# Performance work log

Measured on AMD Instinct MI355X. Metric: run time of the kernel, lower is better.

## Reference

```python
import jax, jax.numpy as jnp
import numpy as np

NUM_GRAPHS = 2048
NODES_PER_GRAPH = 16
EDGES_PER_GRAPH = 128
HEADS = 2
IN_CH = 256
HID_CH = 256
OUT_CH = 256
NEG_SLOPE = 0.2


def setup_inputs() -> dict:
    key = jax.random.key(0)
    ks = jax.random.split(key, 16)
    N = NUM_GRAPHS * NODES_PER_GRAPH
    E = NUM_GRAPHS * EDGES_PER_GRAPH
    x = jax.random.normal(ks[0], (N, IN_CH), dtype=jnp.float32)
    # intra-graph random edges: local indices + per-graph offsets
    offs = jnp.repeat(jnp.arange(NUM_GRAPHS, dtype=jnp.int64) * NODES_PER_GRAPH, EDGES_PER_GRAPH)
    src = jax.random.randint(ks[1], (E,), 0, NODES_PER_GRAPH, dtype=jnp.int64) + offs
    dst = jax.random.randint(ks[2], (E,), 0, NODES_PER_GRAPH, dtype=jnp.int64) + offs
    edge_index = jnp.stack([src, dst], axis=0)
    batch = jnp.repeat(jnp.arange(NUM_GRAPHS, dtype=jnp.int64), NODES_PER_GRAPH)
    s = 0.05
    return {
        'x': x,
        'edge_index': edge_index,
        'batch': batch,
        'W1': jax.random.normal(ks[3], (HEADS * HID_CH, IN_CH), dtype=jnp.float32) * s,
        'att_src1': jax.random.normal(ks[4], (HEADS, HID_CH), dtype=jnp.float32) * s,
        'att_dst1': jax.random.normal(ks[5], (HEADS, HID_CH), dtype=jnp.float32) * s,
        'b1': jax.random.normal(ks[6], (HID_CH,), dtype=jnp.float32) * s,
        'W2': jax.random.normal(ks[7], (HEADS * OUT_CH, HID_CH), dtype=jnp.float32) * s,
        'att_src2': jax.random.normal(ks[8], (HEADS, OUT_CH), dtype=jnp.float32) * s,
        'att_dst2': jax.random.normal(ks[9], (HEADS, OUT_CH), dtype=jnp.float32) * s,
        'b2': jax.random.normal(ks[10], (OUT_CH,), dtype=jnp.float32) * s,
        'w_att': jax.random.normal(ks[11], (OUT_CH, 1), dtype=jnp.float32) * s,
        'b_att': jax.random.normal(ks[12], (1,), dtype=jnp.float32) * s,
        'Wc': jax.random.normal(ks[13], (2, OUT_CH), dtype=jnp.float32) * s,
        'bc': jax.random.normal(ks[14], (2,), dtype=jnp.float32) * s,
    }


def _segment_softmax(logits, seg, num_seg):
    m = jax.ops.segment_max(logits, seg, num_segments=num_seg)
    e = jnp.exp(logits - m[seg])
    s = jax.ops.segment_sum(e, seg, num_segments=num_seg)
    return e / (s[seg] + 1e-16)


def _gat_conv(x, edge_index, W, a_src, a_dst, bias, out_ch):
    # PyG GATConv, heads=HEADS, concat=False, add_self_loops=True
    N = x.shape[0]
    h = (x @ W.T).reshape(N, HEADS, out_ch)              # [N,H,C]
    loop = jnp.arange(N, dtype=edge_index.dtype)
    src = jnp.concatenate([edge_index[0], loop])
    dst = jnp.concatenate([edge_index[1], loop])
    a_s = jnp.einsum('nhc,hc->nh', h, a_src)             # [N,H]
    a_d = jnp.einsum('nhc,hc->nh', h, a_dst)
    alpha = jax.nn.leaky_relu(a_s[src] + a_d[dst], NEG_SLOPE)  # [Etot,H]
    alpha = _segment_softmax(alpha, dst, N)
    msg = alpha[:, :, None] * h[src]                     # [Etot,H,C]
    out = jax.ops.segment_sum(msg, dst, num_segments=N)  # [N,H,C]
    return out.mean(axis=1) + bias                       # concat=False -> mean heads


def reference(x, edge_index, batch, W1, att_src1, att_dst1, b1,
              W2, att_src2, att_dst2, b2, w_att, b_att, Wc, bc):
    num_graphs = NUM_GRAPHS
    h = _gat_conv(x, edge_index, W1, att_src1, att_dst1, b1, HID_CH)
    h = jax.nn.relu(h)
    h = _gat_conv(h, edge_index, W2, att_src2, att_dst2, b2, OUT_CH)
    # per-graph softmax attention pooling (AttentionTemporalLayer per graph)
    logits = (h @ w_att + b_att)[:, 0]                   # [N]
    w = _segment_softmax(logits, batch, num_graphs)      # [N]
    pooled = jax.ops.segment_sum(w[:, None] * h, batch, num_segments=num_graphs)  # [G,OUT]
    return pooled @ Wc.T + bc                            # [G,2]
```

## Files before the change

kernel.cpp:

```cpp
#include <hip/hip_runtime.h>
#include <hip/hip_bf16.h>


#define NGRAPH 2048
#define NPG    16
#define EPG    128
#define ETOT   (EPG + NPG)
#define NNODES (NGRAPH * NPG)
#define NEDGE  (NGRAPH * EPG)
#define CH     256
#define HC     512
#define NEG    0.2f

#define KTILES 12

typedef __attribute__((ext_vector_type(8))) short bf16x8;
typedef __attribute__((ext_vector_type(4))) float f32x4;

__device__ __forceinline__ ushort f2bf(float f) {
    uint u = __float_as_uint(f);
    u += 0x7fffu + ((u >> 16) & 1u);
    return (ushort)(u >> 16);
}
__device__ __forceinline__ float bf2f(ushort b) {
    return __uint_as_float(((uint)b) << 16);
}

__device__ __forceinline__ void gll16(const void* g, void* l) {
    __builtin_amdgcn_global_load_lds(
        (const __attribute__((address_space(1))) unsigned int*)g,
        (__attribute__((address_space(3))) unsigned int*)l, 16, 0, 0);
}

__global__ __launch_bounds__(256) void convert_split(
    const float* __restrict__ src, ushort* __restrict__ dst, int rows)
{
    int i = blockIdx.x * 256 + threadIdx.x;
    if (i >= rows * 64) return;
    int r = i >> 6, c4 = (i & 63) << 2;
    float4 v = *(const float4*)&src[(size_t)r * 256 + c4];
    float vv[4] = {v.x, v.y, v.z, v.w};
    ushort4 hi, lo;
    ushort* hp = (ushort*)&hi; ushort* lp = (ushort*)&lo;
    #pragma unroll
    for (int q = 0; q < 4; ++q) {
        hp[q] = f2bf(vv[q]);
        lp[q] = f2bf(vv[q] - bf2f(hp[q]));
    }
    *(ushort4*)&dst[(size_t)r * 512 + c4]       = hi;
    *(ushort4*)&dst[(size_t)r * 512 + 256 + c4] = lo;
}

__global__ __launch_bounds__(512, 2) void gemm_split(
    const ushort* __restrict__ A2, const ushort* __restrict__ B2,
    float* __restrict__ C)
{
    __shared__ ushort Ash[2 * 256 * 64];
    __shared__ ushort Bsh[2 * 256 * 64];

    const int t  = threadIdx.x;
    const int w  = t >> 6, l = t & 63;
    const int wm = w >> 2, wn = w & 3;
    const int lr = l & 15;
    const int lk = l >> 4;

    const int work = (blockIdx.x & 7) * 32 + (blockIdx.x >> 3);
    const int bn = (work & 1) << 8;
    const int bm = (work >> 1) << 8;

    f32x4 acc[8][4];
    #pragma unroll
    for (int i = 0; i < 8; ++i)
        #pragma unroll
        for (int j = 0; j < 4; ++j)
            acc[i][j] = (f32x4){0.f, 0.f, 0.f, 0.f};

    auto stage = [&](int kt, int buf) {
        const int p    = kt >> 2;
        const int kk   = (kt & 3) << 6;
        const int aoff = ((p == 1) ? 256 : 0) + kk;
        const int boff = ((p == 2) ? 256 : 0) + kk;
        ushort* ab = Ash + buf * (256 * 64);
        ushort* bb = Bsh + buf * (256 * 64);
        #pragma unroll
        for (int i = 0; i < 4; ++i) {
            const int ci = i * 512 + t;
            const int r  = ci >> 3;
            const int cc = (ci & 7) << 3;
            gll16(A2 + (size_t)(bm + r) * 512 + aoff + cc, ab + ci * 8);
            gll16(B2 + (size_t)(bn + r) * 512 + boff + cc, bb + ci * 8);
        }
    };

    stage(0, 0);
    __syncthreads();
    for (int kt = 0; kt < KTILES; ++kt) {
        if (kt + 1 < KTILES) stage(kt + 1, (kt + 1) & 1);
        const ushort* ab = Ash + (kt & 1) * (256 * 64);
        const ushort* bb = Bsh + (kt & 1) * (256 * 64);
        #pragma unroll
        for (int ks = 0; ks < 2; ++ks) {
            bf16x8 af[8], bfr[4];
            #pragma unroll
            for (int mf = 0; mf < 8; ++mf)
                af[mf] = *(const bf16x8*)&ab[(wm * 128 + mf * 16 + lr) * 64 + ks * 32 + lk * 8];
            #pragma unroll
            for (int nf = 0; nf < 4; ++nf)
                bfr[nf] = *(const bf16x8*)&bb[(wn * 64 + nf * 16 + lr) * 64 + ks * 32 + lk * 8];
            #pragma unroll
            for (int mf = 0; mf < 8; ++mf)
                #pragma unroll
                for (int nf = 0; nf < 4; ++nf)
                    acc[mf][nf] = __builtin_amdgcn_mfma_f32_16x16x32_bf16(
                        af[mf], bfr[nf], acc[mf][nf], 0, 0, 0);
        }
        __syncthreads();
    }

    #pragma unroll
    for (int mf = 0; mf < 8; ++mf) {
        const int row = bm + wm * 128 + mf * 16 + lk * 4;
        #pragma unroll
        for (int nf = 0; nf < 4; ++nf) {
            const int col = bn + wn * 64 + nf * 16 + lr;
            float* cp = C + (size_t)row * 512 + col;
            #pragma unroll
            for (int q = 0; q < 4; ++q) cp[(size_t)q * 512] = acc[mf][nf][q];
        }
    }
}

__global__ __launch_bounds__(256) void gat_aggregate(
    const float* __restrict__ hpre,
    const int* __restrict__ src_g, const int* __restrict__ dst_g,
    const float* __restrict__ att_src_g, const float* __restrict__ att_dst_g,
    const float* __restrict__ bias_g,
    float* __restrict__ outf, ushort* __restrict__ outs, int mode)
{
    __shared__ float  hsh[NPG][HC];
    __shared__ float  asd[NPG][2][2];
    __shared__ float  elog[ETOT][2];
    __shared__ int    esrc[ETOT], edst_[ETOT];
    __shared__ int    cnt[NPG + 1];
    __shared__ int    off[NPG];
    __shared__ int    sordr[ETOT];
    __shared__ int    ssrc[ETOT];
    __shared__ float2 salpha[ETOT];

    const int g = blockIdx.x;
    const int t = threadIdx.x;
    const int w = t >> 6, l = t & 63;
    const int nbase = g * NPG;

    {
        const float4* hp = (const float4*)(hpre + (size_t)nbase * HC);
        float4* hs = (float4*)hsh;
        #pragma unroll
        for (int i = 0; i < 8; ++i) hs[t + i * 256] = hp[t + i * 256];
    }
    if (t < EPG) {
        esrc[t]  = src_g[(size_t)g * EPG + t] - nbase;
        edst_[t] = dst_g[(size_t)g * EPG + t] - nbase;
    } else if (t < ETOT) {
        int i = t - EPG;
        esrc[t] = i; edst_[t] = i;
    }
    if (t < NPG + 1) cnt[t] = 0;
    __syncthreads();

    {
        const float4 as0 = *(const float4*)&att_src_g[4 * l];
        const float4 as1 = *(const float4*)&att_src_g[CH + 4 * l];
        const float4 ad0 = *(const float4*)&att_dst_g[4 * l];
        const float4 ad1 = *(const float4*)&att_dst_g[CH + 4 * l];
        for (int nn = w; nn < NPG; nn += 4) {
            float4 h0 = *(const float4*)&hsh[nn][4 * l];
            float4 h1 = *(const float4*)&hsh[nn][CH + 4 * l];
            float s0 = h0.x * as0.x + h0.y * as0.y + h0.z * as0.z + h0.w * as0.w;
            float s1 = h1.x * as1.x + h1.y * as1.y + h1.z * as1.z + h1.w * as1.w;
            float d0 = h0.x * ad0.x + h0.y * ad0.y + h0.z * ad0.z + h0.w * ad0.w;
            float d1 = h1.x * ad1.x + h1.y * ad1.y + h1.z * ad1.z + h1.w * ad1.w;
            #pragma unroll
            for (int o = 1; o < 64; o <<= 1) {
                s0 += __shfl_xor(s0, o); s1 += __shfl_xor(s1, o);
                d0 += __shfl_xor(d0, o); d1 += __shfl_xor(d1, o);
            }
            if (l == 0) {
                asd[nn][0][0] = s0; asd[nn][1][0] = s1;
                asd[nn][0][1] = d0; asd[nn][1][1] = d1;
            }
        }
    }
    if (t < ETOT) atomicAdd(&cnt[edst_[t]], 1);
    __syncthreads();

    for (int idx = t; idx < ETOT * 2; idx += 256) {
        int e = idx >> 1, hh = idx & 1;
        float lg = asd[esrc[e]][hh][0] + asd[edst_[e]][hh][1];
        elog[e][hh] = (lg > 0.f) ? lg : NEG * lg;
    }
    if (t == 0) {
        int s = 0;
        #pragma unroll
        for (int i = 0; i < NPG; ++i) { int c = cnt[i]; cnt[i] = s; s += c; }
        cnt[NPG] = s;
    }
    __syncthreads();
    if (t < NPG) off[t] = cnt[t];
    __syncthreads();
    if (t < ETOT) { int p = atomicAdd(&off[edst_[t]], 1); sordr[p] = t; }
    __syncthreads();

    if (t < NPG * 2) {
        int n = t >> 1, hh = t & 1;
        int b0 = cnt[n], b1 = cnt[n + 1];
        float m = -1e30f;
        for (int i = b0; i < b1; ++i) m = fmaxf(m, elog[sordr[i]][hh]);
        float s = 0.f;
        for (int i = b0; i < b1; ++i) s += expf(elog[sordr[i]][hh] - m);
        float inv = 1.0f / (s + 1e-16f);
        for (int i = b0; i < b1; ++i) {
            int e = sordr[i];
            elog[e][hh] = expf(elog[e][hh] - m) * inv;
        }
    }
    __syncthreads();
    if (t < ETOT) {
        int e = sordr[t];
        ssrc[t]   = esrc[e];
        salpha[t] = make_float2(elog[e][0], elog[e][1]);
    }
    __syncthreads();

    const float4 bi = *(const float4*)&bias_g[4 * l];
    for (int nn = w; nn < NPG; nn += 4) {
        float4 a0 = make_float4(0.f, 0.f, 0.f, 0.f);
        float4 a1 = make_float4(0.f, 0.f, 0.f, 0.f);
        const int b0 = cnt[nn], b1 = cnt[nn + 1];
        for (int i = b0; i < b1; ++i) {
            int s = ssrc[i];
            float2 al = salpha[i];
            float4 h0 = *(const float4*)&hsh[s][4 * l];
            float4 h1 = *(const float4*)&hsh[s][CH + 4 * l];
            a0.x += al.x * h0.x; a0.y += al.x * h0.y;
            a0.z += al.x * h0.z; a0.w += al.x * h0.w;
            a1.x += al.y * h1.x; a1.y += al.y * h1.y;
            a1.z += al.y * h1.z; a1.w += al.y * h1.w;
        }
        float o0 = 0.5f * (a0.x + a1.x) + bi.x;
        float o1 = 0.5f * (a0.y + a1.y) + bi.y;
        float o2 = 0.5f * (a0.z + a1.z) + bi.z;
        float o3 = 0.5f * (a0.w + a1.w) + bi.w;
        if (mode) {
            float v0 = fmaxf(o0, 0.f), v1 = fmaxf(o1, 0.f);
            float v2 = fmaxf(o2, 0.f), v3 = fmaxf(o3, 0.f);
            ushort4 hi, lo;
            hi.x = f2bf(v0); hi.y = f2bf(v1); hi.z = f2bf(v2); hi.w = f2bf(v3);
            lo.x = f2bf(v0 - bf2f(hi.x)); lo.y = f2bf(v1 - bf2f(hi.y));
            lo.z = f2bf(v2 - bf2f(hi.z)); lo.w = f2bf(v3 - bf2f(hi.w));
            ushort* dst = outs + (size_t)(nbase + nn) * 512;
            *(ushort4*)&dst[4 * l]      = hi;
            *(ushort4*)&dst[CH + 4 * l] = lo;
        } else {
            float* dst = outf + (size_t)(nbase + nn) * 256;
            *(float4*)&dst[4 * l] = make_float4(o0, o1, o2, o3);
        }
    }
}

__global__ __launch_bounds__(256) void pool_classify(
    const float* __restrict__ h2,
    const float* __restrict__ w_att, const float* __restrict__ b_att,
    const float* __restrict__ Wc, const float* __restrict__ bc,
    float* __restrict__ outp)
{
    __shared__ float hsh[NPG][CH];
    __shared__ float wsh[CH];
    __shared__ float logit[NPG];
    __shared__ float red[16];

    const int g = blockIdx.x;
    const int t = threadIdx.x;

    const float4* hp = (const float4*)(h2 + (size_t)g * NPG * CH);
    float4* hs = (float4*)hsh;
    for (int i = t; i < NPG * CH / 4; i += 256) hs[i] = hp[i];
    if (t < 64) ((float4*)wsh)[t] = ((const float4*)w_att)[t];
    __syncthreads();

    {
        int n = t >> 4, sub = t & 15;
        float p = 0.f;
        const float* hv = hsh[n];
        #pragma unroll 4
        for (int c = sub * 16; c < sub * 16 + 16; ++c) p += hv[c] * wsh[c];
        p += __shfl_xor(p, 1); p += __shfl_xor(p, 2);
        p += __shfl_xor(p, 4); p += __shfl_xor(p, 8);
        if (sub == 0) logit[n] = p + b_att[0];
    }
    __syncthreads();

    float m = -1e30f;
    #pragma unroll
    for (int i = 0; i < NPG; ++i) m = fmaxf(m, logit[i]);
    float ssum = 0.f;
    #pragma unroll
    for (int i = 0; i < NPG; ++i) ssum += expf(logit[i] - m);
    float inv = 1.0f / (ssum + 1e-16f);

    float pooled = 0.f;
    #pragma unroll
    for (int n = 0; n < NPG; ++n)
        pooled += expf(logit[n] - m) * inv * hsh[n][t];

    float p0 = pooled * Wc[t];
    float p1 = pooled * Wc[CH + t];
    #pragma unroll
    for (int o = 32; o; o >>= 1) {
        p0 += __shfl_xor(p0, o);
        p1 += __shfl_xor(p1, o);
    }
    const int w = t >> 6, l = t & 63;
    if (l == 0) { red[w] = p0; red[8 + w] = p1; }
    __syncthreads();
    if (t == 0) {
        outp[(size_t)g * 2 + 0] = red[0] + red[1] + red[2] + red[3] + bc[0];
        outp[(size_t)g * 2 + 1] = red[8] + red[9] + red[10] + red[11] + bc[1];
    }
}

extern "C" void kernel_launch(void* const* d_in, const int* in_sizes, int n_in,
                              void* d_out, int out_size, void* d_ws, size_t ws_size,
                              hipStream_t stream)
{
    (void)in_sizes; (void)n_in; (void)out_size; (void)ws_size;
    const float* x    = (const float*)d_in[0];
    const int*   ei   = (const int*)d_in[1];
    const float* W1   = (const float*)d_in[3];
    const float* as1  = (const float*)d_in[4];
    const float* ad1  = (const float*)d_in[5];
    const float* b1   = (const float*)d_in[6];
    const float* W2   = (const float*)d_in[7];
    const float* as2  = (const float*)d_in[8];
    const float* ad2  = (const float*)d_in[9];
    const float* b2   = (const float*)d_in[10];
    const float* watt = (const float*)d_in[11];
    const float* batt = (const float*)d_in[12];
    const float* Wc   = (const float*)d_in[13];
    const float* bc   = (const float*)d_in[14];
    float* out = (float*)d_out;

    const int* esrcp = ei;
    const int* edstp = ei + NEDGE;

    const size_t MB = 1024 * 1024;
    ushort* bufA = (ushort*)d_ws;
    float*  hpre = (float*)((char*)d_ws + 32 * MB);
    ushort* w1s  = (ushort*)((char*)d_ws + 96 * MB);
    ushort* w2s  = w1s + 512 * 512;
    float*  h2   = (float*)bufA;

    convert_split<<<dim3(NNODES * 64 / 256), 256, 0, stream>>>(x, bufA, NNODES);
    convert_split<<<dim3(512 * 64 / 256), 256, 0, stream>>>(W1, w1s, 512);
    convert_split<<<dim3(512 * 64 / 256), 256, 0, stream>>>(W2, w2s, 512);

    gemm_split<<<dim3(256), 512, 0, stream>>>(bufA, w1s, hpre);
    gat_aggregate<<<NGRAPH, 256, 0, stream>>>(hpre, esrcp, edstp, as1, ad1, b1,
                                              nullptr, bufA, 1);
    gemm_split<<<dim3(256), 512, 0, stream>>>(bufA, w2s, hpre);
    gat_aggregate<<<NGRAPH, 256, 0, stream>>>(hpre, esrcp, edstp, as2, ad2, b2,
                                              h2, nullptr, 0);
    pool_classify<<<NGRAPH, 256, 0, stream>>>(h2, watt, batt, Wc, bc, out);
}
```

Baseline: 280.4 us.

## Parallelize GAT edge softmax with atomic max/sum and restructure attention dot products

The per-node attention score dot products now use all 256 threads, 16 lanes per node with a 16-wide shuffle reduce, in place of 4 waves looping over nodes. The segment softmax, previously computed serially by 32 threads, is now edge-parallel: an atomicMax on an order-preserving float key gives the max and a shared atomicAdd gives the sum, with normalization folded into the final gather. The serial prefix scan becomes a parallel per-thread scan, and the aggregation loop prefetches the next source index and weight. This removes syncs and serial work in the latency-bound setup of each graph block, at the cost of shared-memory atomics and a summation order that is no longer deterministic.

```diff
diff --git a/kernel.cpp b/kernel.cpp
--- a/kernel.cpp
+++ b/kernel.cpp
@@ -24,6 +24,14 @@
 }
 __device__ __forceinline__ float bf2f(ushort b) {
     return __uint_as_float(((uint)b) << 16);
+}
+__device__ __forceinline__ uint fkey(float f) {
+    uint u = __float_as_uint(f);
+    return u ^ (uint)(((int)u >> 31) | (int)0x80000000u);
+}
+__device__ __forceinline__ float funkey(uint k) {
+    uint u = (k & 0x80000000u) ? (k ^ 0x80000000u) : ~k;
+    return __uint_as_float(u);
 }
 
 __device__ __forceinline__ void gll16(const void* g, void* l) {
@@ -146,6 +154,8 @@
     __shared__ int    sordr[ETOT];
     __shared__ int    ssrc[ETOT];
     __shared__ float2 salpha[ETOT];
+    __shared__ uint   mkey[NPG][2];
+    __shared__ float  ssum[NPG][2];
 
     const int g = blockIdx.x;
     const int t = threadIdx.x;
@@ -166,29 +176,34 @@
         esrc[t] = i; edst_[t] = i;
     }
     if (t < NPG + 1) cnt[t] = 0;
+    if (t < NPG * 2) { ((uint*)mkey)[t] = 0u; ((float*)ssum)[t] = 0.f; }
     __syncthreads();
 
     {
-        const float4 as0 = *(const float4*)&att_src_g[4 * l];
-        const float4 as1 = *(const float4*)&att_src_g[CH + 4 * l];
-        const float4 ad0 = *(const float4*)&att_dst_g[4 * l];
-        const float4 ad1 = *(const float4*)&att_dst_g[CH + 4 * l];
-        for (int nn = w; nn < NPG; nn += 4) {
-            float4 h0 = *(const float4*)&hsh[nn][4 * l];
-            float4 h1 = *(const float4*)&hsh[nn][CH + 4 * l];
-            float s0 = h0.x * as0.x + h0.y * as0.y + h0.z * as0.z + h0.w * as0.w;
-            float s1 = h1.x * as1.x + h1.y * as1.y + h1.z * as1.z + h1.w * as1.w;
-            float d0 = h0.x * ad0.x + h0.y * ad0.y + h0.z * ad0.z + h0.w * ad0.w;
-            float d1 = h1.x * ad1.x + h1.y * ad1.y + h1.z * ad1.z + h1.w * ad1.w;
-            #pragma unroll
-            for (int o = 1; o < 64; o <<= 1) {
-                s0 += __shfl_xor(s0, o); s1 += __shfl_xor(s1, o);
-                d0 += __shfl_xor(d0, o); d1 += __shfl_xor(d1, o);
-            }
-            if (l == 0) {
-                asd[nn][0][0] = s0; asd[nn][1][0] = s1;
-                asd[nn][0][1] = d0; asd[nn][1][1] = d1;
-            }
+        const int n = t >> 4, s = t & 15;
+        float s0 = 0.f, s1 = 0.f, d0 = 0.f, d1 = 0.f;
+        #pragma unroll
+        for (int j = 0; j < 4; ++j) {
+            const int c = s * 4 + j * 64;
+            float4 h0 = *(const float4*)&hsh[n][c];
+            float4 h1 = *(const float4*)&hsh[n][CH + c];
+            float4 a0 = *(const float4*)&att_src_g[c];
+            float4 a1 = *(const float4*)&att_src_g[CH + c];
+            float4 b0 = *(const float4*)&att_dst_g[c];
+            float4 b1 = *(const float4*)&att_dst_g[CH + c];
+            s0 += h0.x * a0.x + h0.y * a0.y + h0.z * a0.z + h0.w * a0.w;
+            s1 += h1.x * a1.x + h1.y * a1.y + h1.z * a1.z + h1.w * a1.w;
+            d0 += h0.x * b0.x + h0.y * b0.y + h0.z * b0.z + h0.w * b0.w;
+            d1 += h1.x * b1.x + h1.y * b1.y + h1.z * b1.z + h1.w * b1.w;
+        }
+        #pragma unroll
+        for (int o = 1; o < 16; o <<= 1) {
+            s0 += __shfl_xor(s0, o); s1 += __shfl_xor(s1, o);
+            d0 += __shfl_xor(d0, o); d1 += __shfl_xor(d1, o);
+        }
+        if (s == 0) {
+            asd[n][0][0] = s0; asd[n][1][0] = s1;
+            asd[n][0][1] = d0; asd[n][1][1] = d1;
         }
     }
     if (t < ETOT) atomicAdd(&cnt[edst_[t]], 1);
@@ -197,38 +212,42 @@
     for (int idx = t; idx < ETOT * 2; idx += 256) {
         int e = idx >> 1, hh = idx & 1;
         float lg = asd[esrc[e]][hh][0] + asd[edst_[e]][hh][1];
-        elog[e][hh] = (lg > 0.f) ? lg : NEG * lg;
-    }
-    if (t == 0) {
-        int s = 0;
-        #pragma unroll
-        for (int i = 0; i < NPG; ++i) { int c = cnt[i]; cnt[i] = s; s += c; }
-        cnt[NPG] = s;
-    }
-    __syncthreads();
-    if (t < NPG) off[t] = cnt[t];
-    __syncthreads();
+        lg = (lg > 0.f) ? lg : NEG * lg;
+        elog[e][hh] = lg;
+        atomicMax(&mkey[edst_[e]][hh], fkey(lg));
+    }
+    if (t < NPG) {
+        int excl = 0, own = 0;
+        #pragma unroll
+        for (int j = 0; j < NPG; ++j) {
+            int c = cnt[j];
+            if (j < t) excl += c;
+            if (j == t) own = c;
+        }
+        off[t] = excl;
+        cnt[t] = excl;
+        if (t == NPG - 1) cnt[NPG] = excl + own;
+    }
+    __syncthreads();
+
+    for (int idx = t; idx < ETOT * 2; idx += 256) {
+        int e = idx >> 1, hh = idx & 1;
+        int dn = edst_[e];
+        float m = funkey(mkey[dn][hh]);
+        float a = expf(elog[e][hh] - m);
+        elog[e][hh] = a;
+        atomicAdd(&ssum[dn][hh], a);
+    }
     if (t < ETOT) { int p = atomicAdd(&off[edst_[t]], 1); sordr[p] = t; }
     __syncthreads();
 
-    if (t < NPG * 2) {
-        int n = t >> 1, hh = t & 1;
-        int b0 = cnt[n], b1 = cnt[n + 1];
-        float m = -1e30f;
-        for (int i = b0; i < b1; ++i) m = fmaxf(m, elog[sordr[i]][hh]);
-        float s = 0.f;
-        for (int i = b0; i < b1; ++i) s += expf(elog[sordr[i]][hh] - m);
-        float inv = 1.0f / (s + 1e-16f);
-        for (int i = b0; i < b1; ++i) {
-            int e = sordr[i];
-            elog[e][hh] = expf(elog[e][hh] - m) * inv;
-        }
-    }
-    __syncthreads();
     if (t < ETOT) {
         int e = sordr[t];
-        ssrc[t]   = esrc[e];
-        salpha[t] = make_float2(elog[e][0], elog[e][1]);
+        int dn = edst_[e];
+        ssrc[t] = esrc[e];
+        float i0 = 1.0f / (ssum[dn][0] + 1e-16f);
+        float i1 = 1.0f / (ssum[dn][1] + 1e-16f);
+        salpha[t] = make_float2(elog[e][0] * i0, elog[e][1] * i1);
     }
     __syncthreads();
 
@@ -237,9 +256,12 @@
         float4 a0 = make_float4(0.f, 0.f, 0.f, 0.f);
         float4 a1 = make_float4(0.f, 0.f, 0.f, 0.f);
         const int b0 = cnt[nn], b1 = cnt[nn + 1];
+        int    s_nx  = ssrc[b0];
+        float2 al_nx = salpha[b0];
         for (int i = b0; i < b1; ++i) {
-            int s = ssrc[i];
-            float2 al = salpha[i];
+            const int    s  = s_nx;
+            const float2 al = al_nx;
+            if (i + 1 < b1) { s_nx = ssrc[i + 1]; al_nx = salpha[i + 1]; }
             float4 h0 = *(const float4*)&hsh[s][4 * l];
             float4 h1 = *(const float4*)&hsh[s][CH + 4 * l];
             a0.x += al.x * h0.x; a0.y += al.x * h0.y;
```

Result: faster. 267.8 us (-4.5%).
